# Performance work log

Hardware: AMD Instinct MI355X
Metric: run time of the kernel (lower is better)

## Reference

```python
import jax, jax.numpy as jnp
import numpy as np

B, L, U, G, H = 64, 110, 768, 512, 256
WP = WF = 10
NSP = 2
R = 2 * NSP * NSP      # 8 relation types
NB = 30                # RGCN num_bases
FF = 2048              # torch TransformerEncoderLayer default dim_feedforward
TAG = 7
N = B * L
NEG = -1e9


def _build_edges():
    # static windowed edge structure (all dialogues have length L)
    js, ks = [], []
    for j in range(L):
        for k in range(max(0, j - WP), min(L - 1, j + WF) + 1):
            js.append(j); ks.append(k)
    j = np.asarray(js, np.int32); k = np.asarray(ks, np.int32)
    c = (j >= k).astype(np.int32)  # edge_type suffix: '0' if j<k else '1'
    off = (np.arange(B, dtype=np.int32) * L)[:, None]
    src = (j[None, :] + off).reshape(-1)
    dst = (k[None, :] + off).reshape(-1)
    return src, dst, np.tile(k, B), np.tile(c, B)


def _ln(x, g, b):
    m = x.mean(-1, keepdims=True)
    v = ((x - m) ** 2).mean(-1, keepdims=True)
    return (x - m) / jnp.sqrt(v + 1e-5) * g + b


def _core(x, in_proj_w, in_proj_b, out_proj_w, out_proj_b, ln1_g, ln1_b,
          ff1_w, ff1_b, ff2_w, ff2_b, ln2_g, ln2_b, to_w, to_b, att_w,
          rgcn_basis, rgcn_comp, rgcn_root, rgcn_bias,
          gc_rel_w, gc_rel_b, gc_root_w, clf1_w, clf1_b, clf2_w, clf2_b,
          speaker, src, dst, k_local, cflag):
    # --- SeqContext: 1-layer, 1-head post-norm transformer (eval mode) ---
    qkv = x @ in_proj_w.T + in_proj_b
    q, kk, v = jnp.split(qkv, 3, axis=-1)
    attn = jax.nn.softmax(jnp.einsum('bqd,bkd->bqk', q, kk) / jnp.sqrt(jnp.float32(U)), -1)
    a = jnp.einsum('bqk,bkd->bqd', attn, v) @ out_proj_w.T + out_proj_b
    h = _ln(x + a, ln1_g, ln1_b)
    ff = jax.nn.relu(h @ ff1_w.T + ff1_b) @ ff2_w.T + ff2_b
    h = _ln(h + ff, ln2_g, ln2_b)
    feats = h @ to_w.T + to_b                      # (B, L, G) node features

    # --- EdgeAtt: windowed softmax attention, score[j,k] = x_j^T W x_k ---
    scores = jnp.einsum('bjd,de,bke->bjk', feats, att_w, feats)
    rel = jnp.arange(L)[None, :] - jnp.arange(L)[:, None]
    mask = (rel >= -WP) & (rel <= WF)
    alpha = jax.nn.softmax(jnp.where(mask[None], scores, NEG), -1)  # (B, L, L)

    xf = feats.reshape(N, G)
    edge_norm = alpha.reshape(N, L)[src, k_local]   # alpha[b, j, k] per edge

    # --- edge types from speakers: idx = (s1*NSP + s2)*2 + c ---
    sp = speaker.reshape(N)
    etype = (sp[src] * NSP + sp[dst]) * 2 + cflag

    # --- RGCNConv: basis decomposition, per-(node, relation) mean + root ---
    w_rel = jnp.einsum('rb,bgh->rgh', rgcn_comp, rgcn_basis)   # (R, G, H)
    xproj = jnp.einsum('ng,rgh->rnh', xf, w_rel)               # (R, N, H)
    msg = xproj[etype, src]                                    # (E, H)
    seg = dst * R + etype
    cnt = jax.ops.segment_sum(jnp.ones_like(edge_norm), seg, num_segments=N * R)
    msg = msg / jnp.maximum(cnt[seg], 1.0)[:, None]
    h1 = jax.ops.segment_sum(msg, dst, num_segments=N) + xf @ rgcn_root + rgcn_bias

    # --- GraphConv: sum-aggregate edge-weighted neighbors + root ---
    agg = jax.ops.segment_sum(edge_norm[:, None] * h1[src], dst, num_segments=N)
    h2 = agg @ gc_rel_w.T + gc_rel_b + h1 @ gc_root_w.T

    # --- Classifier (dropout inactive in eval) ---
    z = jnp.concatenate([xf, h2], axis=-1)
    return jax.nn.relu(z @ clf1_w.T + clf1_b) @ clf2_w.T + clf2_b  # (N, TAG)


def setup_inputs():
    key = jax.random.key(0)
    ks = jax.random.split(key, 16)
    def rn(i, shape, scale=0.02):
        return jax.random.normal(ks[i], shape, jnp.float32) * scale
    src, dst, k_local, cflag = _build_edges()
    return {
        'x': jax.random.normal(ks[0], (B, L, U), jnp.float32),
        'in_proj_w': rn(1, (3 * U, U)), 'in_proj_b': jnp.zeros((3 * U,), jnp.float32),
        'out_proj_w': rn(2, (U, U)), 'out_proj_b': jnp.zeros((U,), jnp.float32),
        'ln1_g': jnp.ones((U,), jnp.float32), 'ln1_b': jnp.zeros((U,), jnp.float32),
        'ff1_w': rn(3, (FF, U)), 'ff1_b': jnp.zeros((FF,), jnp.float32),
        'ff2_w': rn(4, (U, FF)), 'ff2_b': jnp.zeros((U,), jnp.float32),
        'ln2_g': jnp.ones((U,), jnp.float32), 'ln2_b': jnp.zeros((U,), jnp.float32),
        'to_w': rn(5, (G, U)), 'to_b': jnp.zeros((G,), jnp.float32),
        'att_w': rn(6, (G, G), 2.0 / (G + G)),
        'rgcn_basis': rn(7, (NB, G, H)), 'rgcn_comp': rn(8, (R, NB), 0.2),
        'rgcn_root': rn(9, (G, H)), 'rgcn_bias': jnp.zeros((H,), jnp.float32),
        'gc_rel_w': rn(10, (H, H)), 'gc_rel_b': jnp.zeros((H,), jnp.float32),
        'gc_root_w': rn(11, (H, H)),
        'clf1_w': rn(12, (H, G + H)), 'clf1_b': jnp.zeros((H,), jnp.float32),
        'clf2_w': rn(13, (TAG, H)), 'clf2_b': jnp.zeros((TAG,), jnp.float32),
        'speaker': jax.random.randint(ks[14], (B, L), 0, NSP, jnp.int32),
        'src': jnp.asarray(src), 'dst': jnp.asarray(dst),
        'k_local': jnp.asarray(k_local), 'cflag': jnp.asarray(cflag),
        'length': L,
    }


def reference(x, in_proj_w, in_proj_b, out_proj_w, out_proj_b, ln1_g, ln1_b,
              ff1_w, ff1_b, ff2_w, ff2_b, ln2_g, ln2_b, to_w, to_b, att_w,
              rgcn_basis, rgcn_comp, rgcn_root, rgcn_bias,
              gc_rel_w, gc_rel_b, gc_root_w, clf1_w, clf1_b, clf2_w, clf2_b,
              speaker, src, dst, k_local, cflag, length):
    return _core(x, in_proj_w, in_proj_b, out_proj_w, out_proj_b, ln1_g, ln1_b,
                 ff1_w, ff1_b, ff2_w, ff2_b, ln2_g, ln2_b, to_w, to_b, att_w,
                 rgcn_basis, rgcn_comp, rgcn_root, rgcn_bias,
                 gc_rel_w, gc_rel_b, gc_root_w, clf1_w, clf1_b, clf2_w, clf2_b,
                 speaker, src, dst, k_local, cflag)
```

## Files before the change

### kernel.cpp

```cpp
#include <hip/hip_runtime.h>
#include <hip/hip_bf16.h>
#include <math.h>

#define L_   110
#define B_   64
#define N_   7040
#define U_   768
#define G_   512
#define H_   256
#define FF_  2048
#define EPB_ 2200
#define NC_  2816

typedef __attribute__((ext_vector_type(4))) float f32x4;
typedef __attribute__((ext_vector_type(8))) short bf16x8;

__device__ __forceinline__ ushort f2b(float f) {
  union { __hip_bfloat16 h; ushort u; } cv;
  cv.h = __float2bfloat16(f);
  return cv.u;
}
__device__ __forceinline__ float b2f(ushort u) {
  union { float f; unsigned int i; } cv; cv.i = ((unsigned int)u) << 16; return cv.f;
}

__device__ __forceinline__ int edge_prefix(int j) {
  if (j <= 10)  return j * 11 + (j * (j - 1)) / 2;
  if (j <= 100) return 155 + (j - 10) * 21;
  return 2045 + ((141 - j) * (j - 100)) / 2;
}

struct Segs7 { const float* in[7]; ushort* out[7]; int n4[7]; };

__global__ __launch_bounds__(256)
void cvtprep_kernel(Segs7 s, const float* __restrict__ rb,
                    const float* __restrict__ rel, const float* __restrict__ root,
                    float* __restrict__ bias, ushort* __restrict__ gccat)
{
  const int seg = blockIdx.y;
  if (seg < 7) {
    const int n4 = s.n4[seg];
    const float* __restrict__ in = s.in[seg];
    ushort* __restrict__ out = s.out[seg];
    for (int i = blockIdx.x * 256 + threadIdx.x; i < n4; i += gridDim.x * 256) {
      float4 v = ((const float4*)in)[i];
      ushort4 o;
      o.x = f2b(v.x); o.y = f2b(v.y); o.z = f2b(v.z); o.w = f2b(v.w);
      ((ushort4*)out)[i] = o;
    }
  } else {
    const int i = blockIdx.x * 256 + threadIdx.x;
    if (i < NC_) {
      bias[i] = (i < 2560) ? 0.f : rb[i - 2560];
    } else if (i < NC_ + 65536) {
      const int j = i - NC_;
      const int r = j >> 8, c = j & 255;
      gccat[(size_t)r * 512 + c]       = f2b(rel[j]);
      gccat[(size_t)r * 512 + 256 + c] = f2b(root[j]);
    }
  }
}

__global__ __launch_bounds__(256)
void wrelt_kernel(const float* __restrict__ attw, const float* __restrict__ basis,
                  const float* __restrict__ comp, const float* __restrict__ root,
                  ushort* __restrict__ combw)
{
  const int tx = threadIdx.x & 31, ty = threadIdx.x >> 5;
  __shared__ float t[32][33];
  if (blockIdx.z == 0) {
    const int r0 = blockIdx.y * 32, c0 = blockIdx.x * 32;
    for (int i = ty; i < 32; i += 8)
      t[i][tx] = attw[(size_t)(r0 + i) * 512 + c0 + tx];
    __syncthreads();
    for (int i = ty; i < 32; i += 8)
      combw[(size_t)(c0 + i) * 512 + r0 + tx] = f2b(t[tx][i]);
  } else {
    if (blockIdx.y >= 8) return;
    const int g0 = blockIdx.x * 32, h0 = blockIdx.y * 32;
    __shared__ float cs[240];
    if (threadIdx.x < 240) cs[threadIdx.x] = comp[threadIdx.x];
    for (int i = ty; i < 32; i += 8)
      t[i][tx] = root[(size_t)(g0 + i) * 256 + h0 + tx];
    __syncthreads();
    for (int i = ty; i < 32; i += 8)
      combw[(size_t)(2560 + h0 + i) * 512 + g0 + tx] = f2b(t[tx][i]);
    float acc[8][4] = {};
    for (int bb = 0; bb < 30; ++bb) {
      const float* bp = basis + (size_t)bb * (G_ * H_);
#pragma unroll
      for (int k = 0; k < 4; ++k) {
        float v = bp[(size_t)(g0 + ty + 8 * k) * 256 + h0 + tx];
#pragma unroll
        for (int r = 0; r < 8; ++r) acc[r][k] = fmaf(cs[r * 30 + bb], v, acc[r][k]);
      }
    }
    for (int r = 0; r < 8; ++r) {
      __syncthreads();
#pragma unroll
      for (int k = 0; k < 4; ++k) t[ty + 8 * k][tx] = acc[r][k];
      __syncthreads();
      for (int i = ty; i < 32; i += 8)
        combw[(size_t)(512 + r * 256 + h0 + i) * 512 + g0 + tx] = f2b(t[tx][i]);
    }
  }
}

template<bool BIAS, bool RELU>
__global__ __launch_bounds__(256)
void mgemm_kernel(const ushort* __restrict__ A, const ushort* __restrict__ B,
                  const float* __restrict__ bias, ushort* __restrict__ Cb,
                  int K, int lda, int ldb, int ldc)
{
  __shared__ ushort sA[128 * 64];
  __shared__ ushort sB[128 * 64];
  const int tid = threadIdx.x;
  const int w = tid >> 6, l = tid & 63;

  const int gx = gridDim.x;
  const int nwg = gx * gridDim.y;
  const int lid = blockIdx.y * gx + blockIdx.x;
  const int q = nwg >> 3, r = nwg & 7;
  const int xcd = lid & 7, pos = lid >> 3;
  const int nlid = (xcd < r ? xcd * (q + 1) : r * (q + 1) + (xcd - r) * q) + pos;
  const int m0 = (nlid / gx) * 128, n0 = (nlid % gx) * 128;

  const int srow = l >> 3, sg = l & 7, rbase = w * 32;
  const int wr = w >> 1, wc = w & 1;
  const int lrow = l & 15, lk = l >> 4;
  const int xm = (l & 7) << 4;
  const int kb0 = (lk * 16) ^ xm;
  int aoff[4], boff[4];
#pragma unroll
  for (int i = 0; i < 4; ++i) {
    aoff[i] = (wr * 64 + i * 16 + lrow) * 128 + kb0;
    boff[i] = (wc * 64 + i * 16 + lrow) * 128 + kb0;
  }

  f32x4 acc[4][4];
#pragma unroll
  for (int i = 0; i < 4; ++i)
#pragma unroll
    for (int j = 0; j < 4; ++j) acc[i][j] = (f32x4){0.f, 0.f, 0.f, 0.f};

#define STAGE(k0)                                                              \
  {                                                                            \
    _Pragma("unroll")                                                          \
    for (int i = 0; i < 4; ++i) {                                              \
      const int trow = rbase + i * 8 + srow;                                   \
      const int koff = (sg * 8) ^ ((trow & 7) << 3);                           \
      const ushort* ga = A + (size_t)(m0 + trow) * lda + (k0) + koff;          \
      const ushort* gb = B + (size_t)(n0 + trow) * ldb + (k0) + koff;          \
      __builtin_amdgcn_global_load_lds(                                        \
          (const __attribute__((address_space(1))) void*)ga,                   \
          (__attribute__((address_space(3))) void*)&sA[(rbase + i * 8) * 64],  \
          16, 0, 0);                                                           \
      __builtin_amdgcn_global_load_lds(                                        \
          (const __attribute__((address_space(1))) void*)gb,                   \
          (__attribute__((address_space(3))) void*)&sB[(rbase + i * 8) * 64],  \
          16, 0, 0);                                                           \
    }                                                                          \
  }

  STAGE(0)
  for (int kt = 0;;) {
    __syncthreads();
#pragma unroll
    for (int h = 0; h < 2; ++h) {
      const int hx = h * 64;
      bf16x8 af[4], bfr[4];
#pragma unroll
      for (int i = 0; i < 4; ++i) {
        af[i]  = *(const bf16x8*)&sA[(aoff[i] ^ hx) >> 1];
        bfr[i] = *(const bf16x8*)&sB[(boff[i] ^ hx) >> 1];
      }
#pragma unroll
      for (int mi = 0; mi < 4; ++mi)
#pragma unroll
        for (int ni = 0; ni < 4; ++ni)
          acc[mi][ni] = __builtin_amdgcn_mfma_f32_16x16x32_bf16(
              af[mi], bfr[ni], acc[mi][ni], 0, 0, 0);
    }
    kt += 64;
    if (kt >= K) break;
    __syncthreads();
    STAGE(kt)
  }
#undef STAGE

  const int orow = m0 + wr * 64 + lk * 4;
  const int ocol = n0 + wc * 64 + lrow;
#pragma unroll
  for (int mi = 0; mi < 4; ++mi) {
#pragma unroll
    for (int r2 = 0; r2 < 4; ++r2) {
      const int row = orow + mi * 16 + r2;
#pragma unroll
      for (int ni = 0; ni < 4; ++ni) {
        const int col = ocol + ni * 16;
        float v = acc[mi][ni][r2];
        if constexpr (BIAS) v += bias[col];
        if constexpr (RELU) v = fmaxf(v, 0.f);
        Cb[(size_t)row * ldc + col] = f2b(v);
      }
    }
  }
}

template<bool BIAS, bool RELU>
__global__ __launch_bounds__(256)
void mgemm64_kernel(const ushort* __restrict__ A, const ushort* __restrict__ B,
                    const float* __restrict__ bias, ushort* __restrict__ Cb,
                    int K, int lda, int ldb, int ldc)
{
  __shared__ ushort sA[128 * 64];
  __shared__ ushort sB[64 * 64];
  const int tid = threadIdx.x;
  const int w = tid >> 6, l = tid & 63;

  const int gx = gridDim.x;
  const int nwg = gx * gridDim.y;
  const int lid = blockIdx.y * gx + blockIdx.x;
  const int q = nwg >> 3, r = nwg & 7;
  const int xcd = lid & 7, pos = lid >> 3;
  const int nlid = (xcd < r ? xcd * (q + 1) : r * (q + 1) + (xcd - r) * q) + pos;
  const int m0 = (nlid / gx) * 128, n0 = (nlid % gx) * 64;

  const int srow = l >> 3, sg = l & 7;
  const int lrow = l & 15, lk = l >> 4;
  const int xm = (l & 7) << 4;
  const int kb0 = (lk * 16) ^ xm;
  int aoff[2], boff[4];
#pragma unroll
  for (int i = 0; i < 2; ++i) aoff[i] = (w * 32 + i * 16 + lrow) * 128 + kb0;
#pragma unroll
  for (int i = 0; i < 4; ++i) boff[i] = (i * 16 + lrow) * 128 + kb0;

  f32x4 acc[2][4];
#pragma unroll
  for (int i = 0; i < 2; ++i)
#pragma unroll
    for (int j = 0; j < 4; ++j) acc[i][j] = (f32x4){0.f, 0.f, 0.f, 0.f};

#define STAGE64(k0)                                                            \
  {                                                                            \
    _Pragma("unroll")                                                          \
    for (int i = 0; i < 4; ++i) {                                              \
      const int trow = w * 32 + i * 8 + srow;                                  \
      const int koff = (sg * 8) ^ ((trow & 7) << 3);                           \
      const ushort* ga = A + (size_t)(m0 + trow) * lda + (k0) + koff;          \
      __builtin_amdgcn_global_load_lds(                                        \
          (const __attribute__((address_space(1))) void*)ga,                   \
          (__attribute__((address_space(3))) void*)&sA[(w * 32 + i * 8) * 64], \
          16, 0, 0);                                                           \
    }                                                                          \
    _Pragma("unroll")                                                          \
    for (int i = 0; i < 2; ++i) {                                              \
      const int trow = w * 16 + i * 8 + srow;                                  \
      const int koff = (sg * 8) ^ ((trow & 7) << 3);                           \
      const ushort* gb = B + (size_t)(n0 + trow) * ldb + (k0) + koff;          \
      __builtin_amdgcn_global_load_lds(                                        \
          (const __attribute__((address_space(1))) void*)gb,                   \
          (__attribute__((address_space(3))) void*)&sB[(w * 16 + i * 8) * 64], \
          16, 0, 0);                                                           \
    }                                                                          \
  }

  STAGE64(0)
  for (int kt = 0;;) {
    __syncthreads();
#pragma unroll
    for (int h = 0; h < 2; ++h) {
      const int hx = h * 64;
      bf16x8 af[2], bfr[4];
#pragma unroll
      for (int i = 0; i < 2; ++i) af[i] = *(const bf16x8*)&sA[(aoff[i] ^ hx) >> 1];
#pragma unroll
      for (int i = 0; i < 4; ++i) bfr[i] = *(const bf16x8*)&sB[(boff[i] ^ hx) >> 1];
#pragma unroll
      for (int mi = 0; mi < 2; ++mi)
#pragma unroll
        for (int ni = 0; ni < 4; ++ni)
          acc[mi][ni] = __builtin_amdgcn_mfma_f32_16x16x32_bf16(
              af[mi], bfr[ni], acc[mi][ni], 0, 0, 0);
    }
    kt += 64;
    if (kt >= K) break;
    __syncthreads();
    STAGE64(kt)
  }
#undef STAGE64

  const int orow = m0 + w * 32 + lk * 4;
  const int ocol = n0 + lrow;
#pragma unroll
  for (int mi = 0; mi < 2; ++mi) {
#pragma unroll
    for (int r2 = 0; r2 < 4; ++r2) {
      const int row = orow + mi * 16 + r2;
#pragma unroll
      for (int ni = 0; ni < 4; ++ni) {
        const int col = ocol + ni * 16;
        float v = acc[mi][ni][r2];
        if constexpr (BIAS) v += bias[col];
        if constexpr (RELU) v = fmaxf(v, 0.f);
        Cb[(size_t)row * ldc + col] = f2b(v);
      }
    }
  }
}

__global__ __launch_bounds__(256)
void vtrans_kernel(const ushort* __restrict__ qkvb, ushort* __restrict__ vt)
{
  __shared__ ushort t[32][34];
  const int b = blockIdx.z;
  const int r0 = blockIdx.y * 32;
  const int c0 = blockIdx.x * 32;
  const int tid = threadIdx.x;
  for (int e = tid; e < 512; e += 256) {
    const int ri = e >> 4, ci2 = (e & 15) * 2;
    ushort2 v = make_ushort2(0, 0);
    if (r0 + ri < L_)
      v = *(const ushort2*)&qkvb[((size_t)(b * L_) + r0 + ri) * 2304 + 1536 + c0 + ci2];
    t[ri][ci2] = v.x; t[ri][ci2 + 1] = v.y;
  }
  __syncthreads();
  for (int e = tid; e < 512; e += 256) {
    const int ci = e >> 4, ri2 = (e & 15) * 2;
    ushort2 o = make_ushort2(t[ri2][ci], t[ri2 + 1][ci]);
    *(ushort2*)&vt[((size_t)b * 768 + c0 + ci) * 128 + r0 + ri2] = o;
  }
}

__global__ __launch_bounds__(256)
void attnM_kernel(const ushort* __restrict__ qkvb, const ushort* __restrict__ vt,
                  ushort* __restrict__ ctxb)
{
  const int wg = blockIdx.x;
  const int xcd = wg & 7, slot = wg >> 3;
  const int b = xcd * 8 + slot / 7;
  const int qr0 = (slot % 7) * 16;
  const int tid = threadIdx.x, w = tid >> 6, l = tid & 63;
  __shared__ float  sS[16 * 128];
  __shared__ ushort sP[16 * 128];
  const int lrow = l & 15, lq = l >> 4;

  const ushort* Qbase = qkvb + ((size_t)(b * L_) + qr0 + lrow) * 2304 + lq * 8;
  f32x4 accS[2] = {{0.f,0.f,0.f,0.f},{0.f,0.f,0.f,0.f}};
  const int nf0 = w * 2;
  for (int k0 = 0; k0 < 768; k0 += 32) {
    bf16x8 aq = *(const bf16x8*)(Qbase + k0);
#pragma unroll
    for (int f = 0; f < 2; ++f) {
      const int nf = nf0 + f;
      if (nf < 7) {
        const ushort* Kp = qkvb + ((size_t)(b * L_) + nf * 16 + lrow) * 2304
                         + 768 + k0 + lq * 8;
        bf16x8 bk = *(const bf16x8*)Kp;
        accS[f] = __builtin_amdgcn_mfma_f32_16x16x32_bf16(aq, bk, accS[f], 0, 0, 0);
      }
    }
  }
  const float scale = 0.03608439182435161f;
#pragma unroll
  for (int f = 0; f < 2; ++f) {
    const int nf = nf0 + f;
    if (nf < 7) {
#pragma unroll
      for (int r = 0; r < 4; ++r)
        sS[(lq * 4 + r) * 128 + nf * 16 + lrow] = accS[f][r] * scale;
    }
  }
  __syncthreads();

  {
    const int row = w * 4 + lq;
    const int c0 = lrow;
    float m = -1e30f;
    for (int c = c0; c < L_; c += 16) m = fmaxf(m, sS[row * 128 + c]);
#pragma unroll
    for (int off = 8; off; off >>= 1) m = fmaxf(m, __shfl_xor(m, off));
    float pv[7];
    float sum = 0.f;
#pragma unroll
    for (int i = 0; i < 7; ++i) {
      const int c = c0 + i * 16;
      float e = (c < L_) ? __expf(sS[row * 128 + c] - m) : 0.f;
      pv[i] = e; sum += e;
    }
#pragma unroll
    for (int off = 8; off; off >>= 1) sum += __shfl_xor(sum, off);
    const float inv = 1.f / sum;
#pragma unroll
    for (int i = 0; i < 8; ++i) {
      const int c = c0 + i * 16;
      ushort pb = (i < 7 && c < L_) ? f2b(pv[i < 7 ? i : 0] * inv) : (ushort)0;
      const int g = (c >> 3) ^ (row & 7);
      sP[row * 128 + g * 8 + (c & 7)] = pb;
    }
  }
  __syncthreads();

  f32x4 accO[12];
#pragma unroll
  for (int i = 0; i < 12; ++i) accO[i] = (f32x4){0.f, 0.f, 0.f, 0.f};
#pragma unroll
  for (int ks = 0; ks < 4; ++ks) {
    const int k = ks * 32 + lq * 8;
    const int g = (k >> 3) ^ (lrow & 7);
    bf16x8 ap = *(const bf16x8*)&sP[lrow * 128 + g * 8];
#pragma unroll
    for (int i = 0; i < 12; ++i) {
      const int col = w * 192 + i * 16 + lrow;
      bf16x8 bv = *(const bf16x8*)(vt + ((size_t)b * 768 + col) * 128 + k);
      accO[i] = __builtin_amdgcn_mfma_f32_16x16x32_bf16(ap, bv, accO[i], 0, 0, 0);
    }
  }
#pragma unroll
  for (int i = 0; i < 12; ++i) {
    const int col = w * 192 + i * 16 + lrow;
#pragma unroll
    for (int r = 0; r < 4; ++r) {
      const int row = qr0 + lq * 4 + r;
      if (row < L_)
        ctxb[((size_t)b * L_ + row) * 768 + col] = f2b(accO[i][r]);
    }
  }
}

__global__ __launch_bounds__(256)
void ln_kernel(const ushort* __restrict__ Ab, const ushort* __restrict__ Bres,
               const float* __restrict__ g, const float* __restrict__ beta,
               ushort* __restrict__ outb)
{
  const int row = blockIdx.x, tid = threadIdx.x;
  const ushort* ap = Ab + (size_t)row * U_;
  const ushort* bp = Bres + (size_t)row * U_;
  float v0 = b2f(ap[tid])       + b2f(bp[tid]);
  float v1 = b2f(ap[tid + 256]) + b2f(bp[tid + 256]);
  float v2 = b2f(ap[tid + 512]) + b2f(bp[tid + 512]);
  float s = v0 + v1 + v2, sq = v0 * v0 + v1 * v1 + v2 * v2;
  __shared__ float red[8];
#pragma unroll
  for (int off = 32; off; off >>= 1) { s += __shfl_xor(s, off); sq += __shfl_xor(sq, off); }
  const int wave = tid >> 6, lane = tid & 63;
  if (lane == 0) { red[wave] = s; red[4 + wave] = sq; }
  __syncthreads();
  if (tid == 0) {
    float ts = red[0] + red[1] + red[2] + red[3];
    float tq = red[4] + red[5] + red[6] + red[7];
    float m = ts * (1.f / 768.f);
    float var = tq * (1.f / 768.f) - m * m;
    red[0] = m; red[1] = 1.f / sqrtf(var + 1e-5f);
  }
  __syncthreads();
  const float m = red[0], inv = red[1];
  ushort* ob = outb + (size_t)row * U_;
  ob[tid]       = f2b((v0 - m) * inv * g[tid]       + beta[tid]);
  ob[tid + 256] = f2b((v1 - m) * inv * g[tid + 256] + beta[tid + 256]);
  ob[tid + 512] = f2b((v2 - m) * inv * g[tid + 512] + beta[tid + 512]);
}

__global__ __launch_bounds__(256)
void graphfront_kernel(const ushort* __restrict__ combo, const ushort* __restrict__ fcat,
                       const int* __restrict__ speaker,
                       ushort* __restrict__ catb, float* __restrict__ edge_norm)
{
  const int tid = threadIdx.x;
  if (blockIdx.x < N_ / 8) {
    const int n = blockIdx.x * 8 + (tid >> 5);
    const int lane = tid & 31;
    const int b = n / L_, k = n - b * L_;
    const int j0 = max(0, k - 10), j1 = min(L_ - 1, k + 10);
    const int spk = speaker[n];
    float inv[4];
    {
      int cn[4] = {0, 0, 0, 0};
      for (int j = j0; j <= j1; ++j)
        cn[speaker[b * L_ + j] * 2 + (j >= k ? 1 : 0)]++;
#pragma unroll
      for (int q = 0; q < 4; ++q) inv[q] = cn[q] ? 1.f / (float)cn[q] : 0.f;
    }
    float acc[8] = {};
    for (int j = j0; j <= j1; ++j) {
      const int spj = speaker[b * L_ + j];
      const int c = (j >= k) ? 1 : 0;
      const int et = (spj * 2 + spk) * 2 + c;
      const float w = inv[spj * 2 + c];
      bf16x8 v = *(const bf16x8*)&combo[(size_t)(b * L_ + j) * NC_ + 512 + et * 256 + lane * 8];
#pragma unroll
      for (int i = 0; i < 8; ++i) acc[i] = fmaf(b2f((ushort)v[i]), w, acc[i]);
    }
    bf16x8 rt = *(const bf16x8*)&combo[(size_t)n * NC_ + 2560 + lane * 8];
    bf16x8 o;
#pragma unroll
    for (int i = 0; i < 8; ++i) o[i] = (short)f2b(acc[i] + b2f((ushort)rt[i]));
    *(bf16x8*)&catb[(size_t)n * 512 + 256 + lane * 8] = o;
  } else {
    const int bj = blockIdx.x - N_ / 8;
    const int b = bj / L_, j = bj - b * L_;
    const int k0 = max(0, j - 10), k1 = min(L_ - 1, j + 10);
    __shared__ float s[32];
    const int wave = tid >> 6, lane = tid & 63;
    float tr[8];
    {
      bf16x8 tv = *(const bf16x8*)&combo[(size_t)bj * NC_ + lane * 8];
#pragma unroll
      for (int i = 0; i < 8; ++i) tr[i] = b2f((ushort)tv[i]);
    }
    for (int k = k0 + wave; k <= k1; k += 4) {
      bf16x8 v = *(const bf16x8*)&fcat[(size_t)(b * L_ + k) * 768 + lane * 8];
      float sc = 0.f;
#pragma unroll
      for (int i = 0; i < 8; ++i) sc = fmaf(b2f((ushort)v[i]), tr[i], sc);
#pragma unroll
      for (int off = 32; off; off >>= 1) sc += __shfl_xor(sc, off);
      if (lane == 0) s[k - k0] = sc;
    }
    __syncthreads();
    if (tid == 0) {
      const int W = k1 - k0 + 1;
      float m = -1e30f;
      for (int t = 0; t < W; ++t) m = fmaxf(m, s[t]);
      float sum = 0.f;
      for (int t = 0; t < W; ++t) { float e = __expf(s[t] - m); s[t] = e; sum += e; }
      const float inv = 1.f / sum;
      const int base = b * EPB_ + edge_prefix(j);
      for (int t = 0; t < W; ++t) edge_norm[base + t] = s[t] * inv;
    }
  }
}

__global__ __launch_bounds__(256)
void gcn_gather2_kernel(const float* __restrict__ edge_norm,
                        ushort* __restrict__ catb)
{
  const int tid = threadIdx.x;
  const int n = blockIdx.x * 8 + (tid >> 5);
  const int lane = tid & 31;
  const int b = n / L_, k = n - b * L_;
  const int j0 = max(0, k - 10), j1 = min(L_ - 1, k + 10);
  float acc[8] = {};
  for (int j = j0; j <= j1; ++j) {
    const float w = edge_norm[b * EPB_ + edge_prefix(j) + (k - max(0, j - 10))];
    bf16x8 v = *(const bf16x8*)&catb[(size_t)(b * L_ + j) * 512 + 256 + lane * 8];
#pragma unroll
    for (int i = 0; i < 8; ++i) acc[i] = fmaf(b2f((ushort)v[i]), w, acc[i]);
  }
  bf16x8 o;
#pragma unroll
  for (int i = 0; i < 8; ++i) o[i] = (short)f2b(acc[i]);
  *(bf16x8*)&catb[(size_t)n * 512 + lane * 8] = o;
}

__global__ __launch_bounds__(256)
void clf2_kernel(const ushort* __restrict__ hid, const float* __restrict__ w,
                 const float* __restrict__ bias, float* __restrict__ out)
{
  __shared__ float wsm[7 * H_];
  const int tid = threadIdx.x;
  for (int i = tid; i < 7 * H_; i += 256) wsm[i] = w[i];
  __syncthreads();
  const int idx = blockIdx.x * 256 + threadIdx.x;
  if (idx < N_ * 7) {
    const int n = idx / 7, t = idx - n * 7;
    const ushort* hp = hid + (size_t)n * H_;
    const float* wp = wsm + t * H_;
    float acc = bias[t];
    for (int d0 = 0; d0 < H_; d0 += 8) {
      bf16x8 v = *(const bf16x8*)(hp + d0);
#pragma unroll
      for (int i = 0; i < 8; ++i) acc = fmaf(b2f((ushort)v[i]), wp[d0 + i], acc);
    }
    out[idx] = acc;
  }
}

extern "C" void kernel_launch(void* const* d_in, const int* in_sizes, int n_in,
                              void* d_out, int out_size, void* d_ws, size_t ws_size,
                              hipStream_t stream)
{
  const float* x          = (const float*)d_in[0];
  const float* in_proj_w  = (const float*)d_in[1];
  const float* in_proj_b  = (const float*)d_in[2];
  const float* out_proj_w = (const float*)d_in[3];
  const float* out_proj_b = (const float*)d_in[4];
  const float* ln1_g      = (const float*)d_in[5];
  const float* ln1_b      = (const float*)d_in[6];
  const float* ff1_w      = (const float*)d_in[7];
  const float* ff1_b      = (const float*)d_in[8];
  const float* ff2_w      = (const float*)d_in[9];
  const float* ff2_b      = (const float*)d_in[10];
  const float* ln2_g      = (const float*)d_in[11];
  const float* ln2_b      = (const float*)d_in[12];
  const float* to_w       = (const float*)d_in[13];
  const float* to_b       = (const float*)d_in[14];
  const float* att_w      = (const float*)d_in[15];
  const float* rgcn_basis = (const float*)d_in[16];
  const float* rgcn_comp  = (const float*)d_in[17];
  const float* rgcn_root  = (const float*)d_in[18];
  const float* rgcn_bias  = (const float*)d_in[19];
  const float* gc_rel_w   = (const float*)d_in[20];
  const float* gc_rel_b   = (const float*)d_in[21];
  const float* gc_root_w  = (const float*)d_in[22];
  const float* clf1_w     = (const float*)d_in[23];
  const float* clf1_b     = (const float*)d_in[24];
  const float* clf2_w     = (const float*)d_in[25];
  const float* clf2_b     = (const float*)d_in[26];
  const int*   speaker    = (const int*)d_in[27];
  float* out = (float*)d_out;
  char* p = (char*)d_ws;

  ushort* R1b    = (ushort*)p;
  p += (size_t)N_ * 2304 * 4;
  ushort* aprojB = (ushort*)p;
  ushort* ffoB   = aprojB;
  float*  en     = (float*)(p + (size_t)N_ * 512 * 4);
  p += (size_t)N_ * 768 * 4;
  ushort* vt    = (ushort*)p;
  ushort* hidB  = (ushort*)p;
  p += (size_t)N_ * 768 * 4;
  ushort* xb    = (ushort*)p;
  p += (size_t)N_ * 768 * 2;
  ushort* hb    = (ushort*)p;
  ushort* catb  = hb;
  p += (size_t)N_ * 768 * 2;
  ushort* fcat  = (ushort*)p;
  ushort* ctxb  = fcat;
  p += (size_t)N_ * 768 * 2;
  ushort* in_projb = (ushort*)p; p += (size_t)2304 * 768 * 2;
  ushort* out_projb= (ushort*)p; p += (size_t)768 * 768 * 2;
  ushort* ff1b     = (ushort*)p; p += (size_t)2048 * 768 * 2;
  ushort* ff2b     = (ushort*)p; p += (size_t)768 * 2048 * 2;
  ushort* tob      = (ushort*)p; p += (size_t)512 * 768 * 2;
  ushort* combw    = (ushort*)p; p += (size_t)NC_ * 512 * 2;
  ushort* gccat    = (ushort*)p; p += (size_t)256 * 512 * 2;
  ushort* clf1b16  = (ushort*)p; p += (size_t)256 * 768 * 2;
  float*  bias_comb= (float*)p;  p += NC_ * 4;

  Segs7 segs;
  segs.in[0] = x;          segs.out[0] = xb;        segs.n4[0] = N_ * 768 / 4;
  segs.in[1] = in_proj_w;  segs.out[1] = in_projb;  segs.n4[1] = 2304 * 768 / 4;
  segs.in[2] = out_proj_w; segs.out[2] = out_projb; segs.n4[2] = 768 * 768 / 4;
  segs.in[3] = ff1_w;      segs.out[3] = ff1b;      segs.n4[3] = 2048 * 768 / 4;
  segs.in[4] = ff2_w;      segs.out[4] = ff2b;      segs.n4[4] = 768 * 2048 / 4;
  segs.in[5] = to_w;       segs.out[5] = tob;       segs.n4[5] = 512 * 768 / 4;
  segs.in[6] = clf1_w;     segs.out[6] = clf1b16;   segs.n4[6] = 256 * 768 / 4;
  cvtprep_kernel<<<dim3(768, 8), 256, 0, stream>>>(
      segs, rgcn_bias, gc_rel_w, gc_root_w, bias_comb, gccat);
  wrelt_kernel<<<dim3(16, 16, 2), 256, 0, stream>>>(
      att_w, rgcn_basis, rgcn_comp, rgcn_root, combw);

  mgemm_kernel<true, false><<<dim3(18, 55), 256, 0, stream>>>(
      xb, in_projb, in_proj_b, R1b, 768, 768, 768, 2304);
  vtrans_kernel<<<dim3(24, 4, 64), 256, 0, stream>>>(R1b, vt);
  attnM_kernel<<<448, 256, 0, stream>>>(R1b, vt, ctxb);
  mgemm64_kernel<true, false><<<dim3(12, 55), 256, 0, stream>>>(
      ctxb, out_projb, out_proj_b, aprojB, 768, 768, 768, 768);
  ln_kernel<<<N_, 256, 0, stream>>>(xb, aprojB, ln1_g, ln1_b, hb);
  mgemm_kernel<true, true><<<dim3(16, 55), 256, 0, stream>>>(
      hb, ff1b, ff1_b, R1b, 768, 768, 768, 2048);
  mgemm64_kernel<true, false><<<dim3(12, 55), 256, 0, stream>>>(
      R1b, ff2b, ff2_b, ffoB, 2048, 2048, 2048, 768);
  ln_kernel<<<N_, 256, 0, stream>>>(hb, ffoB, ln2_g, ln2_b, hb);
  mgemm64_kernel<true, false><<<dim3(8, 55), 256, 0, stream>>>(
      hb, tob, to_b, fcat, 768, 768, 768, 768);
  mgemm_kernel<true, false><<<dim3(22, 55), 256, 0, stream>>>(
      fcat, combw, bias_comb, R1b, 512, 768, 512, NC_);
  graphfront_kernel<<<N_ / 8 + N_, 256, 0, stream>>>(R1b, fcat, speaker, catb, en);
  gcn_gather2_kernel<<<N_ / 8, 256, 0, stream>>>(en, catb);
  mgemm64_kernel<true, false><<<dim3(4, 55), 256, 0, stream>>>(
      catb, gccat, gc_rel_b, fcat + 512, 512, 512, 512, 768);
  mgemm64_kernel<true, true><<<dim3(4, 55), 256, 0, stream>>>(
      fcat, clf1b16, clf1_b, hidB, 768, 768, 768, 256);
  clf2_kernel<<<(N_ * 7 + 255) / 256, 256, 0, stream>>>(hidB, clf2_w, clf2_b, out);
}
```

Measured before the change: 300.7 us.

## Fuse out-proj and LayerNorm into attention; fold GraphConv weights into classifier

The attention kernel now keeps the context tile in shared memory, does the out-projection with MFMA, and applies residual plus LayerNorm in place. This removes the separate out-proj GEMM, the LN kernel and the context round-trip through global memory. The GraphConv linear layer is folded algebraically into the first classifier weights: a small GEMM builds a combined weight and a folded bias at prep time. The classifier then reads a 1024-wide concatenated buffer, removing one GEMM launch. The two prep kernels are merged into one. The risk is a heavier attention kernel, with more LDS and registers and lower occupancy, and a change in bf16 rounding from the folded weights.

Measured after the change: 354.7 us. +18.0%, slower.

```diff
diff --git a/kernel.cpp b/kernel.cpp
--- a/kernel.cpp
+++ b/kernel.cpp
@@ -30,78 +30,92 @@
   return 2045 + ((141 - j) * (j - 100)) / 2;
 }
 
-struct Segs7 { const float* in[7]; ushort* out[7]; int n4[7]; };
-
-__global__ __launch_bounds__(256)
-void cvtprep_kernel(Segs7 s, const float* __restrict__ rb,
-                    const float* __restrict__ rel, const float* __restrict__ root,
-                    float* __restrict__ bias, ushort* __restrict__ gccat)
-{
-  const int seg = blockIdx.y;
-  if (seg < 7) {
-    const int n4 = s.n4[seg];
-    const float* __restrict__ in = s.in[seg];
-    ushort* __restrict__ out = s.out[seg];
-    for (int i = blockIdx.x * 256 + threadIdx.x; i < n4; i += gridDim.x * 256) {
+struct PrepArgs {
+  const float* cin[7]; ushort* cout[7]; int n4[7];
+  const float* rb; const float* grel; const float* groot;
+  const float* clf1w; const float* clf1bias; const float* grelb;
+  const float* attw; const float* basis; const float* comp; const float* root;
+  float* bias_comb; ushort* grelrootT; ushort* Wp; float* bias2; ushort* combw;
+};
+
+__global__ __launch_bounds__(256)
+void prep_kernel(PrepArgs a)
+{
+  __shared__ float t[32][33];
+  __shared__ float cs[240];
+  const int y = blockIdx.y;
+  const int tid = threadIdx.x;
+  if (y < 7) {
+    const int n4 = a.n4[y];
+    const float* __restrict__ in = a.cin[y];
+    ushort* __restrict__ out = a.cout[y];
+    for (int i = blockIdx.x * 256 + tid; i < n4; i += gridDim.x * 256) {
       float4 v = ((const float4*)in)[i];
       ushort4 o;
       o.x = f2b(v.x); o.y = f2b(v.y); o.z = f2b(v.z); o.w = f2b(v.w);
       ((ushort4*)out)[i] = o;
     }
+  } else if (y == 7) {
+    const int total = NC_ + 65536 + 65536 + 131072 + 256;
+    for (int i = blockIdx.x * 256 + tid; i < total; i += gridDim.x * 256) {
+      if (i < NC_) {
+        a.bias_comb[i] = (i < 2560) ? 0.f : a.rb[i - 2560];
+      } else if (i < NC_ + 65536) {
+        const int j = i - NC_;
+        const int k = j >> 8, c = j & 255;
+        a.grelrootT[(size_t)c * 256 + k] = f2b(a.grel[j]);
+      } else if (i < NC_ + 131072) {
+        const int j = i - NC_ - 65536;
+        const int k = j >> 8, c = j & 255;
+        a.grelrootT[(size_t)(256 + c) * 256 + k] = f2b(a.groot[j]);
+      } else if (i < NC_ + 131072 + 131072) {
+        const int j = i - NC_ - 131072;
+        const int o = j >> 9, c = j & 511;
+        a.Wp[(size_t)o * 1024 + c] = f2b(a.clf1w[(size_t)o * 768 + c]);
+      } else {
+        const int tt = i - (NC_ + 131072 + 131072);
+        float s = a.clf1bias[tt];
+        for (int k = 0; k < 256; ++k)
+          s = fmaf(a.clf1w[(size_t)tt * 768 + 512 + k], a.grelb[k], s);
+        a.bias2[tt] = s;
+      }
+    }
   } else {
-    const int i = blockIdx.x * 256 + threadIdx.x;
-    if (i < NC_) {
-      bias[i] = (i < 2560) ? 0.f : rb[i - 2560];
-    } else if (i < NC_ + 65536) {
-      const int j = i - NC_;
-      const int r = j >> 8, c = j & 255;
-      gccat[(size_t)r * 512 + c]       = f2b(rel[j]);
-      gccat[(size_t)r * 512 + 256 + c] = f2b(root[j]);
-    }
-  }
-}
-
-__global__ __launch_bounds__(256)
-void wrelt_kernel(const float* __restrict__ attw, const float* __restrict__ basis,
-                  const float* __restrict__ comp, const float* __restrict__ root,
-                  ushort* __restrict__ combw)
-{
-  const int tx = threadIdx.x & 31, ty = threadIdx.x >> 5;
-  __shared__ float t[32][33];
-  if (blockIdx.z == 0) {
-    const int r0 = blockIdx.y * 32, c0 = blockIdx.x * 32;
-    for (int i = ty; i < 32; i += 8)
-      t[i][tx] = attw[(size_t)(r0 + i) * 512 + c0 + tx];
-    __syncthreads();
-    for (int i = ty; i < 32; i += 8)
-      combw[(size_t)(c0 + i) * 512 + r0 + tx] = f2b(t[tx][i]);
-  } else {
-    if (blockIdx.y >= 8) return;
-    const int g0 = blockIdx.x * 32, h0 = blockIdx.y * 32;
-    __shared__ float cs[240];
-    if (threadIdx.x < 240) cs[threadIdx.x] = comp[threadIdx.x];
-    for (int i = ty; i < 32; i += 8)
-      t[i][tx] = root[(size_t)(g0 + i) * 256 + h0 + tx];
-    __syncthreads();
-    for (int i = ty; i < 32; i += 8)
-      combw[(size_t)(2560 + h0 + i) * 512 + g0 + tx] = f2b(t[tx][i]);
-    float acc[8][4] = {};
-    for (int bb = 0; bb < 30; ++bb) {
-      const float* bp = basis + (size_t)bb * (G_ * H_);
-#pragma unroll
-      for (int k = 0; k < 4; ++k) {
-        float v = bp[(size_t)(g0 + ty + 8 * k) * 256 + h0 + tx];
-#pragma unroll
-        for (int r = 0; r < 8; ++r) acc[r][k] = fmaf(cs[r * 30 + bb], v, acc[r][k]);
-      }
-    }
-    for (int r = 0; r < 8; ++r) {
-      __syncthreads();
-#pragma unroll
-      for (int k = 0; k < 4; ++k) t[ty + 8 * k][tx] = acc[r][k];
+    const int tx = tid & 31, ty = tid >> 5;
+    if (blockIdx.x < 256) {
+      const int r0 = (blockIdx.x >> 4) * 32, c0 = (blockIdx.x & 15) * 32;
+      for (int i = ty; i < 32; i += 8)
+        t[i][tx] = a.attw[(size_t)(r0 + i) * 512 + c0 + tx];
       __syncthreads();
       for (int i = ty; i < 32; i += 8)
-        combw[(size_t)(512 + r * 256 + h0 + i) * 512 + g0 + tx] = f2b(t[tx][i]);
+        a.combw[(size_t)(c0 + i) * 512 + r0 + tx] = f2b(t[tx][i]);
+    } else if (blockIdx.x < 384) {
+      const int t2 = blockIdx.x - 256;
+      const int g0 = (t2 & 15) * 32, h0 = (t2 >> 4) * 32;
+      if (tid < 240) cs[tid] = a.comp[tid];
+      for (int i = ty; i < 32; i += 8)
+        t[i][tx] = a.root[(size_t)(g0 + i) * 256 + h0 + tx];
+      __syncthreads();
+      for (int i = ty; i < 32; i += 8)
+        a.combw[(size_t)(2560 + h0 + i) * 512 + g0 + tx] = f2b(t[tx][i]);
+      float acc[8][4] = {};
+      for (int bb = 0; bb < 30; ++bb) {
+        const float* bp = a.basis + (size_t)bb * (G_ * H_);
+#pragma unroll
+        for (int k = 0; k < 4; ++k) {
+          float v = bp[(size_t)(g0 + ty + 8 * k) * 256 + h0 + tx];
+#pragma unroll
+          for (int r = 0; r < 8; ++r) acc[r][k] = fmaf(cs[r * 30 + bb], v, acc[r][k]);
+        }
+      }
+      for (int r = 0; r < 8; ++r) {
+        __syncthreads();
+#pragma unroll
+        for (int k = 0; k < 4; ++k) t[ty + 8 * k][tx] = acc[r][k];
+        __syncthreads();
+        for (int i = ty; i < 32; i += 8)
+          a.combw[(size_t)(512 + r * 256 + h0 + i) * 512 + g0 + tx] = f2b(t[tx][i]);
+      }
     }
   }
 }
@@ -334,8 +348,10 @@
 }
 
 __global__ __launch_bounds__(256)
-void attnM_kernel(const ushort* __restrict__ qkvb, const ushort* __restrict__ vt,
-                  ushort* __restrict__ ctxb)
+void attnF_kernel(const ushort* __restrict__ qkvb, const ushort* __restrict__ vt,
+                  const ushort* __restrict__ xb, const ushort* __restrict__ opw,
+                  const float* __restrict__ opb, const float* __restrict__ g1,
+                  const float* __restrict__ b1, ushort* __restrict__ hb)
 {
   const int wg = blockIdx.x;
   const int xcd = wg & 7, slot = wg >> 3;
@@ -344,6 +360,9 @@
   const int tid = threadIdx.x, w = tid >> 6, l = tid & 63;
   __shared__ float  sS[16 * 128];
   __shared__ ushort sP[16 * 128];
+  __shared__ ushort sC[16][776];
+  __shared__ float  sRed[16][8];
+  __shared__ float  sMean[16], sRstd[16];
   const int lrow = l & 15, lq = l >> 4;
 
   const ushort* Qbase = qkvb + ((size_t)(b * L_) + qr0 + lrow) * 2304 + lq * 8;
@@ -421,10 +440,81 @@
   for (int i = 0; i < 12; ++i) {
     const int col = w * 192 + i * 16 + lrow;
 #pragma unroll
+    for (int r = 0; r < 4; ++r)
+      sC[lq * 4 + r][col] = f2b(accO[i][r]);
+  }
+  __syncthreads();
+
+  f32x4 acc2[12];
+#pragma unroll
+  for (int i = 0; i < 12; ++i) acc2[i] = (f32x4){0.f, 0.f, 0.f, 0.f};
+  for (int k0 = 0; k0 < 768; k0 += 32) {
+    bf16x8 af = *(const bf16x8*)&sC[lrow][k0 + lq * 8];
+#pragma unroll
+    for (int i = 0; i < 12; ++i) {
+      const int col = w * 192 + i * 16 + lrow;
+      bf16x8 bfr = *(const bf16x8*)(opw + (size_t)col * 768 + k0 + lq * 8);
+      acc2[i] = __builtin_amdgcn_mfma_f32_16x16x32_bf16(af, bfr, acc2[i], 0, 0, 0);
+    }
+  }
+
+  float vv[12][4];
+  bool rv[4];
+#pragma unroll
+  for (int r = 0; r < 4; ++r) rv[r] = (qr0 + lq * 4 + r) < L_;
+  float ssum[4] = {0.f, 0.f, 0.f, 0.f}, ssq[4] = {0.f, 0.f, 0.f, 0.f};
+#pragma unroll
+  for (int i = 0; i < 12; ++i) {
+    const int col = w * 192 + i * 16 + lrow;
+    const float bb = opb[col];
+#pragma unroll
     for (int r = 0; r < 4; ++r) {
-      const int row = qr0 + lq * 4 + r;
-      if (row < L_)
-        ctxb[((size_t)b * L_ + row) * 768 + col] = f2b(accO[i][r]);
+      float xv = 0.f;
+      if (rv[r]) {
+        const size_t grow = (size_t)(b * L_ + qr0 + lq * 4 + r);
+        xv = b2f(xb[grow * 768 + col]);
+      }
+      float v = acc2[i][r] + bb + xv;
+      vv[i][r] = v;
+      ssum[r] += v; ssq[r] += v * v;
+    }
+  }
+#pragma unroll
+  for (int off = 1; off < 16; off <<= 1) {
+#pragma unroll
+    for (int r = 0; r < 4; ++r) {
+      ssum[r] += __shfl_xor(ssum[r], off);
+      ssq[r]  += __shfl_xor(ssq[r], off);
+    }
+  }
+  if (lrow == 0) {
+#pragma unroll
+    for (int r = 0; r < 4; ++r) {
+      sRed[lq * 4 + r][w] = ssum[r];
+      sRed[lq * 4 + r][4 + w] = ssq[r];
+    }
+  }
+  __syncthreads();
+  if (tid < 16) {
+    float S = sRed[tid][0] + sRed[tid][1] + sRed[tid][2] + sRed[tid][3];
+    float Q = sRed[tid][4] + sRed[tid][5] + sRed[tid][6] + sRed[tid][7];
+    float mn = S * (1.f / 768.f);
+    float var = Q * (1.f / 768.f) - mn * mn;
+    sMean[tid] = mn;
+    sRstd[tid] = rsqrtf(var + 1e-5f);
+  }
+  __syncthreads();
+#pragma unroll
+  for (int i = 0; i < 12; ++i) {
+    const int col = w * 192 + i * 16 + lrow;
+    const float gg = g1[col], b2 = b1[col];
+#pragma unroll
+    for (int r = 0; r < 4; ++r) {
+      if (rv[r]) {
+        const int lr = lq * 4 + r;
+        const size_t grow = (size_t)(b * L_ + qr0 + lr);
+        hb[grow * 768 + col] = f2b((vv[i][r] - sMean[lr]) * sRstd[lr] * gg + b2);
+      }
     }
   }
 }
@@ -463,9 +553,8 @@
 }
 
 __global__ __launch_bounds__(256)
-void graphfront_kernel(const ushort* __restrict__ combo, const ushort* __restrict__ fcat,
-                       const int* __restrict__ speaker,
-                       ushort* __restrict__ catb, float* __restrict__ edge_norm)
+void graphfront_kernel(const ushort* __restrict__ combo, ushort* __restrict__ fcat2,
+                       const int* __restrict__ speaker, float* __restrict__ edge_norm)
 {
   const int tid = threadIdx.x;
   if (blockIdx.x < N_ / 8) {
@@ -496,7 +585,7 @@
     bf16x8 o;
 #pragma unroll
     for (int i = 0; i < 8; ++i) o[i] = (short)f2b(acc[i] + b2f((ushort)rt[i]));
-    *(bf16x8*)&catb[(size_t)n * 512 + 256 + lane * 8] = o;
+    *(bf16x8*)&fcat2[(size_t)n * 1024 + 768 + lane * 8] = o;
   } else {
     const int bj = blockIdx.x - N_ / 8;
     const int b = bj / L_, j = bj - b * L_;
@@ -510,7 +599,7 @@
       for (int i = 0; i < 8; ++i) tr[i] = b2f((ushort)tv[i]);
     }
     for (int k = k0 + wave; k <= k1; k += 4) {
-      bf16x8 v = *(const bf16x8*)&fcat[(size_t)(b * L_ + k) * 768 + lane * 8];
+      bf16x8 v = *(const bf16x8*)&fcat2[(size_t)(b * L_ + k) * 1024 + lane * 8];
       float sc = 0.f;
 #pragma unroll
       for (int i = 0; i < 8; ++i) sc = fmaf(b2f((ushort)v[i]), tr[i], sc);
@@ -534,7 +623,7 @@
 
 __global__ __launch_bounds__(256)
 void gcn_gather2_kernel(const float* __restrict__ edge_norm,
-                        ushort* __restrict__ catb)
+                        ushort* __restrict__ fcat2)
 {
   const int tid = threadIdx.x;
   const int n = blockIdx.x * 8 + (tid >> 5);
@@ -544,14 +633,14 @@
   float acc[8] = {};
   for (int j = j0; j <= j1; ++j) {
     const float w = edge_norm[b * EPB_ + edge_prefix(j) + (k - max(0, j - 10))];
-    bf16x8 v = *(const bf16x8*)&catb[(size_t)(b * L_ + j) * 512 + 256 + lane * 8];
+    bf16x8 v = *(const bf16x8*)&fcat2[(size_t)(b * L_ + j) * 1024 + 768 + lane * 8];
 #pragma unroll
     for (int i = 0; i < 8; ++i) acc[i] = fmaf(b2f((ushort)v[i]), w, acc[i]);
   }
   bf16x8 o;
 #pragma unroll
   for (int i = 0; i < 8; ++i) o[i] = (short)f2b(acc[i]);
-  *(bf16x8*)&catb[(size_t)n * 512 + lane * 8] = o;
+  *(bf16x8*)&fcat2[(size_t)n * 1024 + 512 + lane * 8] = o;
 }
 
 __global__ __launch_bounds__(256)
@@ -614,8 +703,7 @@
 
   ushort* R1b    = (ushort*)p;
   p += (size_t)N_ * 2304 * 4;
-  ushort* aprojB = (ushort*)p;
-  ushort* ffoB   = aprojB;
+  ushort* ffoB   = (ushort*)p;
   float*  en     = (float*)(p + (size_t)N_ * 512 * 4);
   p += (size_t)N_ * 768 * 4;
   ushort* vt    = (ushort*)p;
@@ -624,55 +712,55 @@
   ushort* xb    = (ushort*)p;
   p += (size_t)N_ * 768 * 2;
   ushort* hb    = (ushort*)p;
-  ushort* catb  = hb;
   p += (size_t)N_ * 768 * 2;
-  ushort* fcat  = (ushort*)p;
-  ushort* ctxb  = fcat;
-  p += (size_t)N_ * 768 * 2;
+  ushort* fcat2 = (ushort*)p;
+  p += (size_t)N_ * 1024 * 2;
   ushort* in_projb = (ushort*)p; p += (size_t)2304 * 768 * 2;
   ushort* out_projb= (ushort*)p; p += (size_t)768 * 768 * 2;
   ushort* ff1b     = (ushort*)p; p += (size_t)2048 * 768 * 2;
   ushort* ff2b     = (ushort*)p; p += (size_t)768 * 2048 * 2;
   ushort* tob      = (ushort*)p; p += (size_t)512 * 768 * 2;
   ushort* combw    = (ushort*)p; p += (size_t)NC_ * 512 * 2;
-  ushort* gccat    = (ushort*)p; p += (size_t)256 * 512 * 2;
   ushort* clf1b16  = (ushort*)p; p += (size_t)256 * 768 * 2;
+  ushort* Wp       = (ushort*)p; p += (size_t)256 * 1024 * 2;
+  ushort* grelrootT= (ushort*)p; p += (size_t)512 * 256 * 2;
   float*  bias_comb= (float*)p;  p += NC_ * 4;
-
-  Segs7 segs;
-  segs.in[0] = x;          segs.out[0] = xb;        segs.n4[0] = N_ * 768 / 4;
-  segs.in[1] = in_proj_w;  segs.out[1] = in_projb;  segs.n4[1] = 2304 * 768 / 4;
-  segs.in[2] = out_proj_w; segs.out[2] = out_projb; segs.n4[2] = 768 * 768 / 4;
-  segs.in[3] = ff1_w;      segs.out[3] = ff1b;      segs.n4[3] = 2048 * 768 / 4;
-  segs.in[4] = ff2_w;      segs.out[4] = ff2b;      segs.n4[4] = 768 * 2048 / 4;
-  segs.in[5] = to_w;       segs.out[5] = tob;       segs.n4[5] = 512 * 768 / 4;
-  segs.in[6] = clf1_w;     segs.out[6] = clf1b16;   segs.n4[6] = 256 * 768 / 4;
-  cvtprep_kernel<<<dim3(768, 8), 256, 0, stream>>>(
-      segs, rgcn_bias, gc_rel_w, gc_root_w, bias_comb, gccat);
-  wrelt_kernel<<<dim3(16, 16, 2), 256, 0, stream>>>(
-      att_w, rgcn_basis, rgcn_comp, rgcn_root, combw);
+  float*  bias2    = (float*)p;  p += 256 * 4;
+
+  PrepArgs pa;
+  pa.cin[0] = x;          pa.cout[0] = xb;        pa.n4[0] = N_ * 768 / 4;
+  pa.cin[1] = in_proj_w;  pa.cout[1] = in_projb;  pa.n4[1] = 2304 * 768 / 4;
+  pa.cin[2] = out_proj_w; pa.cout[2] = out_projb; pa.n4[2] = 768 * 768 / 4;
+  pa.cin[3] = ff1_w;      pa.cout[3] = ff1b;      pa.n4[3] = 2048 * 768 / 4;
+  pa.cin[4] = ff2_w;      pa.cout[4] = ff2b;      pa.n4[4] = 768 * 2048 / 4;
+  pa.cin[5] = to_w;       pa.cout[5] = tob;       pa.n4[5] = 512 * 768 / 4;
+  pa.cin[6] = clf1_w;     pa.cout[6] = clf1b16;   pa.n4[6] = 256 * 768 / 4;
+  pa.rb = rgcn_bias; pa.grel = gc_rel_w; pa.groot = gc_root_w;
+  pa.clf1w = clf1_w; pa.clf1bias = clf1_b; pa.grelb = gc_rel_b;
+  pa.attw = att_w; pa.basis = rgcn_basis; pa.comp = rgcn_comp; pa.root = rgcn_root;
+  pa.bias_comb = bias_comb; pa.grelrootT = grelrootT; pa.Wp = Wp;
+  pa.bias2 = bias2; pa.combw = combw;
+  prep_kernel<<<dim3(768, 9), 256, 0, stream>>>(pa);
+  mgemm64_kernel<false, false><<<dim3(8, 2), 256, 0, stream>>>(
+      clf1b16 + 512, grelrootT, nullptr, Wp + 512, 256, 768, 256, 1024);
 
   mgemm_kernel<true, false><<<dim3(18, 55), 256, 0, stream>>>(
       xb, in_projb, in_proj_b, R1b, 768, 768, 768, 2304);
   vtrans_kernel<<<dim3(24, 4, 64), 256, 0, stream>>>(R1b, vt);
-  attnM_kernel<<<448, 256, 0, stream>>>(R1b, vt, ctxb);
-  mgemm64_kernel<true, false><<<dim3(12, 55), 256, 0, stream>>>(
-      ctxb, out_projb, out_proj_b, aprojB, 768, 768, 768, 768);
-  ln_kernel<<<N_, 256, 0, stream>>>(xb, aprojB, ln1_g, ln1_b, hb);
+  attnF_kernel<<<448, 256, 0, stream>>>(R1b, vt, xb, out_projb, out_proj_b,
+                                        ln1_g, ln1_b, hb);
   mgemm_kernel<true, true><<<dim3(16, 55), 256, 0, stream>>>(
       hb, ff1b, ff1_b, R1b, 768, 768, 768, 2048);
   mgemm64_kernel<true, false><<<dim3(12, 55), 256, 0, stream>>>(
       R1b, ff2b, ff2_b, ffoB, 2048, 2048, 2048, 768);
   ln_kernel<<<N_, 256, 0, stream>>>(hb, ffoB, ln2_g, ln2_b, hb);
   mgemm64_kernel<true, false><<<dim3(8, 55), 256, 0, stream>>>(
-      hb, tob, to_b, fcat, 768, 768, 768, 768);
+      hb, tob, to_b, fcat2, 768, 768, 768, 1024);
   mgemm_kernel<true, false><<<dim3(22, 55), 256, 0, stream>>>(
-      fcat, combw, bias_comb, R1b, 512, 768, 512, NC_);
-  graphfront_kernel<<<N_ / 8 + N_, 256, 0, stream>>>(R1b, fcat, speaker, catb, en);
-  gcn_gather2_kernel<<<N_ / 8, 256, 0, stream>>>(en, catb);
-  mgemm64_kernel<true, false><<<dim3(4, 55), 256, 0, stream>>>(
-      catb, gccat, gc_rel_b, fcat + 512, 512, 512, 512, 768);
+      fcat2, combw, bias_comb, R1b, 512, 1024, 512, NC_);
+  graphfront_kernel<<<N_ / 8 + N_, 256, 0, stream>>>(R1b, fcat2, speaker, en);
+  gcn_gather2_kernel<<<N_ / 8, 256, 0, stream>>>(en, fcat2);
   mgemm64_kernel<true, true><<<dim3(4, 55), 256, 0, stream>>>(
-      fcat, clf1b16, clf1_b, hidB, 768, 768, 768, 256);
+      fcat2, Wp, bias2, hidB, 1024, 1024, 1024, 256);
   clf2_kernel<<<(N_ * 7 + 255) / 256, 256, 0, stream>>>(hidB, clf2_w, clf2_b, out);
 }
```
